# Kernel optimization log

Measured on AMD Instinct MI355X. Metric: run time of the kernel, lower is better.

Reference implementation:

```python
import math
import jax, jax.numpy as jnp
import numpy as np

MAX_N = 3; MAX_L = 3
CUTOFF = 5.0; TB_CUTOFF = 4.0; NBLOCKS = 3
N_NODES = 5000; N_EDGES = 60000; N_TRIP = 400000
NELEM = 89; DN = 128; DE = 128; UNITS = 128; DEG = MAX_N * MAX_L

# zeros of spherical bessel j_l, l = 0..2, first 3 roots each
J_ROOTS = np.array([
    [3.141592653589793, 6.283185307179586, 9.42477796076938],
    [4.493409457909064, 7.725251836937707, 10.904121659428899],
    [5.763459196894550, 9.095011330476355, 12.322940970566582],
])

def _jl(l, x, xp):
    s, c = xp.sin(x), xp.cos(x)
    if l == 0:
        return s / x
    if l == 1:
        return s / x**2 - c / x
    if l == 2:
        return (3.0 / x**3 - 1.0 / x) * s - 3.0 * c / x**2
    return (15.0 / x**4 - 6.0 / x**2) * s - (15.0 / x**3 - 1.0 / x) * c

SBF_FACTOR = math.sqrt(2.0 / CUTOFF**3)
SBF_NORM = np.stack([np.abs(_jl(l + 1, J_ROOTS[l], np)) for l in range(MAX_L)])  # [3,3]

def sbf_expand(r):  # [n] -> [n, MAX_L*MAX_N], l-major (matches torch cat over l)
    cols = []
    for l in range(MAX_L):
        x = r[:, None] * (J_ROOTS[l] / CUTOFF)[None, :]
        cols.append(_jl(l, x, jnp) * (SBF_FACTOR / SBF_NORM[l])[None, :])
    return jnp.concatenate(cols, axis=1)

Y00 = 0.28209479177387814  # 0.5*sqrt(1/pi)
Y10 = 0.4886025119029199   # sqrt(3/(4pi))
Y20 = 0.31539156525252005  # 0.25*sqrt(5/pi)

def shf_expand(cos_t):  # [n] -> [n, MAX_L]  real Y_l0(theta)
    return jnp.stack([jnp.full_like(cos_t, Y00), Y10 * cos_t, Y20 * (3.0 * cos_t**2 - 1.0)], axis=1)

def poly_cutoff(r, c):
    x = r / c
    return 1.0 - 6.0 * x**5 + 15.0 * x**4 - 10.0 * x**3

def gated_mlp(x, Ws, bs, gWs, gbs):
    h = x
    for W, b in zip(Ws, bs):
        h = jax.nn.silu(h @ W + b)
    g = x
    n = len(gWs)
    for i, (W, b) in enumerate(zip(gWs, gbs)):
        g = g @ W + b
        g = jax.nn.sigmoid(g) if i == n - 1 else jax.nn.silu(g)
    return h * g

def _forward(pos, node_type, src, dst, t_src, t_dst, emb_table, edge_emb_W, edge_emb_b,
             tb_atom_W, tb_atom_b, tb_bond_W, tb_bond_Wg,
             W0, b0, W1, b1, W2, b2, gW0, gb0, gW1, gb1, gW2, gb2, wt,
             fW0, fb0, fW1, fb1, fW2, fb2):
    n_nodes = pos.shape[0]; n_edges = src.shape[0]
    bond_vec = pos[dst] - pos[src]                              # [E,3]
    bond_dist = jnp.sqrt(jnp.sum(bond_vec**2, axis=1) + 1e-12)  # [E]
    rbf = sbf_expand(bond_dist)                                 # [E,9]
    # triplet (line-graph edge) geometry
    v1, v2 = bond_vec[t_src], bond_vec[t_dst]
    cos_t = jnp.sum(v1 * v2, axis=1) / (bond_dist[t_src] * bond_dist[t_dst])
    three_basis = sbf_expand(bond_dist[t_dst]) * jnp.repeat(shf_expand(cos_t), MAX_N, axis=1)  # [T,9]
    cut3 = poly_cutoff(bond_dist, TB_CUTOFF)
    tw = (cut3[t_src] * cut3[t_dst])[:, None]                   # [T,1]
    end_atom = dst[t_dst]                                       # [T]
    node_feat = emb_table[node_type]                            # [N,DN]
    edge_feat = jax.nn.silu(rbf @ edge_emb_W + edge_emb_b)      # [E,DE]
    for k in range(NBLOCKS):
        # --- three-body interaction ---
        atoms = jax.nn.sigmoid(node_feat @ tb_atom_W[k] + tb_atom_b[k])  # [N,9]
        basis = three_basis * atoms[end_atom] * tw                        # [T,9]
        nb = jax.ops.segment_sum(basis, t_src, num_segments=n_edges)      # [E,9]
        edge_feat = edge_feat + jax.nn.silu(nb @ tb_bond_W[k]) * jax.nn.sigmoid(nb @ tb_bond_Wg[k])
        # --- graph conv: edge update ---
        x = jnp.concatenate([node_feat[src], node_feat[dst], edge_feat], axis=1)  # [E,384]
        e_upd = gated_mlp(x, (W0[k, 0], W1[k, 0], W2[k, 0]), (b0[k, 0], b1[k, 0], b2[k, 0]),
                          (gW0[k, 0], gW1[k, 0], gW2[k, 0]), (gb0[k, 0], gb1[k, 0], gb2[k, 0])) * (rbf @ wt[k, 0])
        edge_feat = edge_feat + e_upd
        # --- graph conv: node update (sum messages at destination) ---
        x = jnp.concatenate([node_feat[src], node_feat[dst], edge_feat], axis=1)
        mess = gated_mlp(x, (W0[k, 1], W1[k, 1], W2[k, 1]), (b0[k, 1], b1[k, 1], b2[k, 1]),
                         (gW0[k, 1], gW1[k, 1], gW2[k, 1]), (gb0[k, 1], gb1[k, 1], gb2[k, 1])) * (rbf @ wt[k, 1])
        node_feat = node_feat + jax.ops.segment_sum(mess, dst, num_segments=n_nodes)
    # ReduceReadOut('mean') over nodes (single graph) + final MLP
    v = jnp.mean(node_feat, axis=0)
    h = jax.nn.silu(v @ fW0 + fb0)
    h = jax.nn.silu(h @ fW1 + fb1)
    return jnp.squeeze(h @ fW2 + fb2)

def setup_inputs() -> dict:
    key = jax.random.key(0)
    ks = iter(jax.random.split(key, 64))
    def nrm(shape, fan_in):
        return jax.random.normal(next(ks), shape, dtype=jnp.float32) / math.sqrt(float(fan_in))
    pos = jax.random.normal(next(ks), (N_NODES, 3), dtype=jnp.float32) * 1.5
    node_type = jax.random.randint(next(ks), (N_NODES,), 0, NELEM, dtype=jnp.int32)
    src = jax.random.randint(next(ks), (N_EDGES,), 0, N_NODES, dtype=jnp.int32)
    dst = (src + 1 + jax.random.randint(next(ks), (N_EDGES,), 0, N_NODES - 1, dtype=jnp.int32)) % N_NODES
    t_src = jax.random.randint(next(ks), (N_TRIP,), 0, N_EDGES, dtype=jnp.int32)
    t_dst = jax.random.randint(next(ks), (N_TRIP,), 0, N_EDGES, dtype=jnp.int32)
    DIN = 2 * DN + DE
    z = lambda *s: jnp.zeros(s, jnp.float32)
    return dict(
        pos=pos, node_type=node_type, src=src, dst=dst, t_src=t_src, t_dst=t_dst,
        emb_table=nrm((NELEM, DN), 1.0),
        edge_emb_W=nrm((DEG, DE), DEG), edge_emb_b=z(DE),
        tb_atom_W=nrm((NBLOCKS, DN, DEG), DN), tb_atom_b=z(NBLOCKS, DEG),
        tb_bond_W=nrm((NBLOCKS, DEG, DE), DEG), tb_bond_Wg=nrm((NBLOCKS, DEG, DE), DEG),
        W0=nrm((NBLOCKS, 2, DIN, UNITS), DIN), b0=z(NBLOCKS, 2, UNITS),
        W1=nrm((NBLOCKS, 2, UNITS, UNITS), UNITS), b1=z(NBLOCKS, 2, UNITS),
        W2=nrm((NBLOCKS, 2, UNITS, DE), UNITS), b2=z(NBLOCKS, 2, DE),
        gW0=nrm((NBLOCKS, 2, DIN, UNITS), DIN), gb0=z(NBLOCKS, 2, UNITS),
        gW1=nrm((NBLOCKS, 2, UNITS, UNITS), UNITS), gb1=z(NBLOCKS, 2, UNITS),
        gW2=nrm((NBLOCKS, 2, UNITS, DE), UNITS), gb2=z(NBLOCKS, 2, DE),
        wt=nrm((NBLOCKS, 2, DEG, DE), DEG),
        fW0=nrm((DN, UNITS), DN), fb0=z(UNITS),
        fW1=nrm((UNITS, UNITS), UNITS), fb1=z(UNITS),
        fW2=nrm((UNITS, 1), UNITS), fb2=z(1))

def reference(pos, node_type, src, dst, t_src, t_dst, emb_table, edge_emb_W, edge_emb_b,
              tb_atom_W, tb_atom_b, tb_bond_W, tb_bond_Wg,
              W0, b0, W1, b1, W2, b2, gW0, gb0, gW1, gb1, gW2, gb2, wt,
              fW0, fb0, fW1, fb1, fW2, fb2):
    return _forward(pos, node_type, src, dst, t_src, t_dst, emb_table, edge_emb_W, edge_emb_b,
                    tb_atom_W, tb_atom_b, tb_bond_W, tb_bond_Wg,
                    W0, b0, W1, b1, W2, b2, gW0, gb0, gW1, gb1, gW2, gb2, wt,
                    fW0, fb0, fW1, fb1, fW2, fb2)
```

## Files before the change

### kernel.cpp

```cpp
#include <hip/hip_runtime.h>
#include <stdint.h>

typedef __attribute__((ext_vector_type(8))) short bf16x8;
typedef __attribute__((ext_vector_type(4))) float f32x4;
typedef __attribute__((ext_vector_type(4))) uint32_t u32x4;

#define XSS 408
#define HSS 144
#define TE 32

__device__ __forceinline__ float sigm(float x) { return __fdividef(1.0f, 1.0f + __expf(-x)); }
__device__ __forceinline__ float silu(float x) { return __fdividef(x, 1.0f + __expf(-x)); }
__device__ __forceinline__ short f2bf(float f) {
  uint32_t u = __float_as_uint(f);
  u = (u + 0x7fffu + ((u >> 16) & 1u)) >> 16;
  return (short)u;
}
__device__ __forceinline__ uint32_t cvt2(float lo, float hi) {
  uint32_t d;
  asm("v_cvt_pk_bf16_f32 %0, %1, %2" : "=v"(d) : "v"(lo), "v"(hi));
  return d;
}
__device__ __forceinline__ short f2bf1(float f) { return (short)cvt2(f, f); }

__device__ __forceinline__ float jl_eval(int l, float x) {
  float s, c;
  sincosf(x, &s, &c);
  float ix = 1.0f / x, ix2 = ix * ix;
  if (l == 0) return s * ix;
  if (l == 1) return s * ix2 - c * ix;
  if (l == 2) return (3.0f * ix2 * ix - ix) * s - 3.0f * ix2 * c;
  return (15.0f * ix2 * ix2 - 6.0f * ix2) * s - (15.0f * ix2 * ix - ix) * c;
}

__global__ void setup1_kernel(const int* __restrict__ ntb, const float* __restrict__ emb,
                              float* __restrict__ nf, int N,
                              const float* __restrict__ pos, const int* __restrict__ src,
                              const int* __restrict__ dst, float* __restrict__ bvec,
                              float* __restrict__ bdist, float* __restrict__ rbf,
                              float* __restrict__ cut3, int E,
                              const int* __restrict__ t_src, int* __restrict__ cnt_e,
                              int* __restrict__ cnt_n, int T) {
  int i = blockIdx.x * 256 + threadIdx.x;
  if (i < N * 128) {
    int n = i >> 7, c = i & 127;
    nf[i] = emb[ntb[n] * 128 + c];
  }
  if (i < E) {
    int s = src[i], d = dst[i];
    float dx = pos[d * 3 + 0] - pos[s * 3 + 0];
    float dy = pos[d * 3 + 1] - pos[s * 3 + 1];
    float dz = pos[d * 3 + 2] - pos[s * 3 + 2];
    float r = sqrtf(dx * dx + dy * dy + dz * dz + 1e-12f);
    bvec[i * 3 + 0] = dx; bvec[i * 3 + 1] = dy; bvec[i * 3 + 2] = dz;
    bdist[i] = r;
    const float roots[3][3] = {
        {3.141592653589793f, 6.283185307179586f, 9.42477796076938f},
        {4.493409457909064f, 7.725251836937707f, 10.904121659428899f},
        {5.763459196894550f, 9.095011330476355f, 12.322940970566582f}};
#pragma unroll
    for (int l = 0; l < 3; ++l) {
#pragma unroll
      for (int n = 0; n < 3; ++n) {
        float root = roots[l][n];
        float x = r * (root * 0.2f);
        float norm = fabsf(jl_eval(l + 1, root));
        rbf[i * 9 + l * 3 + n] = jl_eval(l, x) * (0.12649110640673518f / norm);
      }
    }
    float xx = r * 0.25f;
    float x3 = xx * xx * xx;
    cut3[i] = 1.0f - 6.0f * x3 * xx * xx + 15.0f * x3 * xx - 10.0f * x3;
    atomicAdd(&cnt_n[d], 1);
  }
  if (i < T) atomicAdd(&cnt_e[t_src[i]], 1);
}

__device__ void scan_chunk(const int* __restrict__ in, int* __restrict__ incl,
                           int* __restrict__ bsum, int L, int b) {
  __shared__ int sm[256];
  int i = b * 256 + threadIdx.x;
  int v = i < L ? in[i] : 0;
  sm[threadIdx.x] = v;
  __syncthreads();
  for (int st = 1; st < 256; st <<= 1) {
    int t = threadIdx.x >= st ? sm[threadIdx.x - st] : 0;
    __syncthreads();
    sm[threadIdx.x] += t;
    __syncthreads();
  }
  if (i < L) incl[i] = sm[threadIdx.x];
  if (threadIdx.x == 255) bsum[b] = sm[255];
}

__global__ void setup2_kernel(const float* __restrict__ rbf, const float* __restrict__ eW,
                              const float* __restrict__ eB, float* __restrict__ ef, int E,
                              const int* __restrict__ cnt_e, int* __restrict__ incl_e,
                              int* __restrict__ bsum_e, int ebk,
                              const int* __restrict__ cnt_n, int* __restrict__ incl_n,
                              int* __restrict__ bsum_n, int nbk, int N,
                              const float* __restrict__ nf, const float* __restrict__ taW,
                              const float* __restrict__ taB, float* __restrict__ atoms) {
  int b = blockIdx.x;
  if (b < ebk) scan_chunk(cnt_e, incl_e, bsum_e, E, b);
  else if (b < ebk + nbk) scan_chunk(cnt_n, incl_n, bsum_n, N, b - ebk);
  int i = b * 256 + threadIdx.x;
  if (i < E * 128) {
    int e = i >> 7, c = i & 127;
    float acc = eB[c];
#pragma unroll
    for (int d = 0; d < 9; ++d) acc += rbf[e * 9 + d] * eW[d * 128 + c];
    ef[i] = silu(acc);
  }
  if (i < N * 9) {
    int n = i / 9, d = i - n * 9;
    float acc = taB[d];
    for (int c = 0; c < 128; ++c) acc += nf[n * 128 + c] * taW[c * 9 + d];
    atoms[i] = sigm(acc);
  }
}

__global__ void scan_top2_kernel(int* __restrict__ bsum_e, int ne, int* __restrict__ bsum_n,
                                 int nn) {
  __shared__ int sm[1024];
  int* bs = blockIdx.x == 0 ? bsum_e : bsum_n;
  int nb = blockIdx.x == 0 ? ne : nn;
  int tid = threadIdx.x;
  int orig = tid < nb ? bs[tid] : 0;
  sm[tid] = orig;
  __syncthreads();
  for (int st = 1; st < 1024; st <<= 1) {
    int t = tid >= st ? sm[tid - st] : 0;
    __syncthreads();
    sm[tid] += t;
    __syncthreads();
  }
  if (tid < nb) bs[tid] = sm[tid] - orig;
}

__global__ void fin2_kernel(const int* __restrict__ cnt_e, const int* __restrict__ incl_e,
                            const int* __restrict__ bsum_e, int ebk, int* __restrict__ off_e,
                            int* __restrict__ cur_e, int E, const int* __restrict__ cnt_n,
                            const int* __restrict__ incl_n, const int* __restrict__ bsum_n,
                            int* __restrict__ off_n, int* __restrict__ cur_n, int N) {
  int b = blockIdx.x;
  if (b < ebk) {
    int i = b * 256 + threadIdx.x;
    if (i < E) {
      int o = incl_e[i] - cnt_e[i] + bsum_e[b];
      off_e[i] = o; cur_e[i] = o;
    }
  } else {
    int bb = b - ebk;
    int i = bb * 256 + threadIdx.x;
    if (i < N) {
      int o = incl_n[i] - cnt_n[i] + bsum_n[bb];
      off_n[i] = o; cur_n[i] = o;
    }
  }
}

__global__ void build_kernel(const int* __restrict__ t_src, const int* __restrict__ t_dst,
                             const int* __restrict__ dst, const float* __restrict__ bvec,
                             const float* __restrict__ bdist, const float* __restrict__ rbf,
                             const float* __restrict__ cut3, int* __restrict__ cur_e,
                             float* __restrict__ stbp, int* __restrict__ sa, int T,
                             int* __restrict__ cur_n, int* __restrict__ eperm, int E) {
  int t = blockIdx.x * 256 + threadIdx.x;
  if (t < T) {
    int i = t_src[t], j = t_dst[t];
    float ax = bvec[i * 3], ay = bvec[i * 3 + 1], az = bvec[i * 3 + 2];
    float bx = bvec[j * 3], by = bvec[j * 3 + 1], bz = bvec[j * 3 + 2];
    float ct = (ax * bx + ay * by + az * bz) / (bdist[i] * bdist[j]);
    float tw = cut3[i] * cut3[j];
    float sh[3];
    sh[0] = 0.28209479177387814f * tw;
    sh[1] = 0.4886025119029199f * ct * tw;
    sh[2] = 0.31539156525252005f * (3.0f * ct * ct - 1.0f) * tw;
    int pos = atomicAdd(&cur_e[i], 1);
#pragma unroll
    for (int l = 0; l < 3; ++l)
#pragma unroll
      for (int n = 0; n < 3; ++n)
        stbp[(size_t)pos * 9 + l * 3 + n] = rbf[j * 9 + l * 3 + n] * sh[l];
    sa[pos] = dst[j];
  }
  if (t < E) {
    int pos = atomicAdd(&cur_n[dst[t]], 1);
    eperm[pos] = t;
  }
}

__device__ void pack_one(const float* __restrict__ Wf, short* __restrict__ Wp, int K, int rr) {
  int per = 8 * (K / 32) * 64;
  int u = rr / per, r2 = rr - u * per;
  int lane = r2 & 63, tile = r2 >> 6;
  int kt = tile % (K / 32), nt = tile / (K / 32);
  int n = nt * 16 + (lane & 15);
  int k0 = kt * 32 + (lane >> 4) * 8;
  const float* s = Wf + (size_t)u * K * 128;
  bf16x8 v;
#pragma unroll
  for (int e = 0; e < 8; ++e) v[e] = f2bf(s[(size_t)(k0 + e) * 128 + n]);
  *(bf16x8*)(Wp + (size_t)u * K * 128 + (size_t)tile * 512 + lane * 8) = v;
}

__global__ void pack_all_kernel(const float* __restrict__ W0, const float* __restrict__ G0,
                                const float* __restrict__ W1, const float* __restrict__ G1,
                                const float* __restrict__ W2, const float* __restrict__ G2,
                                short* __restrict__ pW0, short* __restrict__ pG0,
                                short* __restrict__ pW1, short* __restrict__ pG1,
                                short* __restrict__ pW2, short* __restrict__ pG2) {
  int idx = blockIdx.x * 256 + threadIdx.x;
  const int t384 = 6 * 8 * 12 * 64, t128 = 6 * 8 * 4 * 64;
  if (idx < t384) pack_one(W0, pW0, 384, idx);
  else if (idx < 2 * t384) pack_one(G0, pG0, 384, idx - t384);
  else {
    int j = idx - 2 * t384;
    if (j < t128) pack_one(W1, pW1, 128, j);
    else if (j < 2 * t128) pack_one(G1, pG1, 128, j - t128);
    else if (j < 3 * t128) pack_one(W2, pW2, 128, j - 2 * t128);
    else if (j < 4 * t128) pack_one(G2, pG2, 128, j - 3 * t128);
  }
}

__device__ __forceinline__ f32x4 mfma16(bf16x8 a, bf16x8 b, f32x4 c) {
  return __builtin_amdgcn_mfma_f32_16x16x32_bf16(a, b, c, 0, 0, 0);
}

__device__ __forceinline__ void store_hg(short* hsb, short* gsb, int wave, int lane,
                                         const f32x4 (&aW)[2], const f32x4 (&aG)[2]) {
  const int lrow = lane & 15, lk = lane >> 4;
  const int colx = (wave * 16 + lrow) ^ (lk << 4);
#pragma unroll
  for (int mt = 0; mt < 2; ++mt)
#pragma unroll
    for (int rg = 0; rg < 4; ++rg) {
      int row = mt * 16 + lk * 4 + rg;
      hsb[row * HSS + colx] = f2bf1(silu(aW[mt][rg]));
      gsb[row * HSS + colx] = f2bf1(silu(aG[mt][rg]));
    }
}

__device__ __forceinline__ void layer128w(const short* hin, const short* gin,
                                          const short* __restrict__ pW,
                                          const short* __restrict__ pG,
                                          const float* __restrict__ Bh,
                                          const float* __restrict__ Bg, int wave, int lane,
                                          f32x4 (&aW)[2], f32x4 (&aG)[2]) {
  const int lrow = lane & 15, lk = lane >> 4;
  const int s0 = (lrow >> 2) & 3;
  float bw = Bh[wave * 16 + lrow], bg = Bg[wave * 16 + lrow];
  aW[0] = {bw, bw, bw, bw}; aW[1] = aW[0];
  aG[0] = {bg, bg, bg, bg}; aG[1] = aG[0];
#pragma unroll
  for (int kt = 0; kt < 4; ++kt) {
    int aoff = (kt * 32 + lk * 8) ^ (s0 << 4);
    bf16x8 ah0 = *(const bf16x8*)(hin + (size_t)lrow * HSS + aoff);
    bf16x8 ah1 = *(const bf16x8*)(hin + (size_t)(16 + lrow) * HSS + aoff);
    bf16x8 ag0 = *(const bf16x8*)(gin + (size_t)lrow * HSS + aoff);
    bf16x8 ag1 = *(const bf16x8*)(gin + (size_t)(16 + lrow) * HSS + aoff);
    bf16x8 bw8 = *(const bf16x8*)(pW + (size_t)(wave * 4 + kt) * 512 + lane * 8);
    bf16x8 bg8 = *(const bf16x8*)(pG + (size_t)(wave * 4 + kt) * 512 + lane * 8);
    aW[0] = mfma16(ah0, bw8, aW[0]);
    aW[1] = mfma16(ah1, bw8, aW[1]);
    aG[0] = mfma16(ag0, bg8, aG[0]);
    aG[1] = mfma16(ag1, bg8, aG[1]);
  }
}

__device__ __forceinline__ void run_chain(
    const short* xsb, short* hsb, short* gsb,
    const short* __restrict__ pW0, const short* __restrict__ pG0,
    const short* __restrict__ pW1, const short* __restrict__ pG1,
    const short* __restrict__ pW2, const short* __restrict__ pG2,
    const float* __restrict__ B0, const float* __restrict__ Gb0,
    const float* __restrict__ B1, const float* __restrict__ Gb1,
    const float* __restrict__ B2, const float* __restrict__ Gb2,
    int wave, int lane, f32x4 (&aW)[2], f32x4 (&aG)[2]) {
  const int lrow = lane & 15, lk = lane >> 4;
  const int s0 = (lrow >> 2) & 3;
  {
    float bw = B0[wave * 16 + lrow], bg = Gb0[wave * 16 + lrow];
    aW[0] = {bw, bw, bw, bw}; aW[1] = aW[0];
    aG[0] = {bg, bg, bg, bg}; aG[1] = aG[0];
  }
#pragma unroll
  for (int kt = 0; kt < 12; ++kt) {
    int al = kt * 32 + lk * 8;
    int aoff = (al < 256) ? al : (256 + ((al - 256) ^ (s0 << 4)));
    bf16x8 a0 = *(const bf16x8*)(xsb + (size_t)lrow * XSS + aoff);
    bf16x8 a1 = *(const bf16x8*)(xsb + (size_t)(16 + lrow) * XSS + aoff);
    bf16x8 bw8 = *(const bf16x8*)(pW0 + (size_t)(wave * 12 + kt) * 512 + lane * 8);
    bf16x8 bg8 = *(const bf16x8*)(pG0 + (size_t)(wave * 12 + kt) * 512 + lane * 8);
    aW[0] = mfma16(a0, bw8, aW[0]);
    aW[1] = mfma16(a1, bw8, aW[1]);
    aG[0] = mfma16(a0, bg8, aG[0]);
    aG[1] = mfma16(a1, bg8, aG[1]);
  }
  store_hg(hsb, gsb, wave, lane, aW, aG);
  __syncthreads();
  layer128w(hsb, gsb, pW1, pG1, B1, Gb1, wave, lane, aW, aG);
  __syncthreads();
  store_hg(hsb, gsb, wave, lane, aW, aG);
  __syncthreads();
  layer128w(hsb, gsb, pW2, pG2, B2, Gb2, wave, lane, aW, aG);
}

__global__ __launch_bounds__(512, 6) void gmlp_fused(
    const float* __restrict__ nf, float* __restrict__ ef, const float* __restrict__ rbf,
    const int* __restrict__ src, const int* __restrict__ dst,
    const float* __restrict__ stbp, const int* __restrict__ sa,
    const int* __restrict__ off_e, const int* __restrict__ cnt_e,
    const float* __restrict__ atoms,
    const float* __restrict__ tbW, const float* __restrict__ tbG,
    const short* __restrict__ pW0a, const short* __restrict__ pG0a,
    const short* __restrict__ pW1a, const short* __restrict__ pG1a,
    const short* __restrict__ pW2a, const short* __restrict__ pG2a,
    const float* __restrict__ B0a, const float* __restrict__ Gb0a,
    const float* __restrict__ B1a, const float* __restrict__ Gb1a,
    const float* __restrict__ B2a, const float* __restrict__ Gb2a,
    const float* __restrict__ WTa,
    const short* __restrict__ pW0b, const short* __restrict__ pG0b,
    const short* __restrict__ pW1b, const short* __restrict__ pG1b,
    const short* __restrict__ pW2b, const short* __restrict__ pG2b,
    const float* __restrict__ B0b, const float* __restrict__ Gb0b,
    const float* __restrict__ B1b, const float* __restrict__ Gb1b,
    const float* __restrict__ B2b, const float* __restrict__ Gb2b,
    const float* __restrict__ WTb,
    float* __restrict__ mbuf, int E) {
  __shared__ __align__(16) short xs[32][XSS];
  __shared__ __align__(16) short hs[32 * HSS];
  __shared__ __align__(16) short gs[32 * HSS];
  __shared__ float rs[32][12];
  __shared__ float nbl[32][12];
  const int tid = threadIdx.x;
  const int e0 = blockIdx.x * TE;
  const int r = tid >> 4, q = tid & 15;
  const int sr = (r >> 2) & 3;
  int eg = e0 + r; if (eg >= E) eg = E - 1;

  if (q < 9) {
    int o = off_e[eg], c = cnt_e[eg];
    float acc = 0.f;
    for (int pp = o; pp < o + c; ++pp)
      acc += stbp[(size_t)pp * 9 + q] * atoms[(size_t)sa[pp] * 9 + q];
    nbl[r][q] = acc;
  }
  {
    const float* sp0 = nf + (size_t)src[eg] * 128;
    const float* sp1 = nf + (size_t)dst[eg] * 128;
#pragma unroll
    for (int seg = 0; seg < 2; ++seg) {
      const float* sp = seg == 0 ? sp0 : sp1;
      float4 f0 = *(const float4*)(sp + q * 8);
      float4 f1 = *(const float4*)(sp + q * 8 + 4);
      u32x4 v = {cvt2(f0.x, f0.y), cvt2(f0.z, f0.w), cvt2(f1.x, f1.y), cvt2(f1.z, f1.w)};
      *(u32x4*)&xs[r][seg * 128 + q * 8] = v;
    }
    for (int idx = tid; idx < 32 * 9; idx += 512) {
      int rr = idx / 9, d = idx - rr * 9;
      int ee = e0 + rr; if (ee >= E) ee = E - 1;
      rs[rr][d] = rbf[ee * 9 + d];
    }
  }
  __syncthreads();

  {
    float nb9[9];
#pragma unroll
    for (int d = 0; d < 9; ++d) nb9[d] = nbl[r][d];
    float fv[8];
    {
      float4 f0 = *(const float4*)(ef + (size_t)eg * 128 + q * 8);
      float4 f1 = *(const float4*)(ef + (size_t)eg * 128 + q * 8 + 4);
      fv[0]=f0.x; fv[1]=f0.y; fv[2]=f0.z; fv[3]=f0.w;
      fv[4]=f1.x; fv[5]=f1.y; fv[6]=f1.z; fv[7]=f1.w;
    }
    float a8[8], b8[8];
#pragma unroll
    for (int c = 0; c < 8; ++c) { a8[c] = 0.f; b8[c] = 0.f; }
#pragma unroll
    for (int d = 0; d < 9; ++d) {
      float nbd = nb9[d];
      float4 w0 = *(const float4*)(tbW + d * 128 + q * 8);
      float4 w1 = *(const float4*)(tbW + d * 128 + q * 8 + 4);
      float4 g0 = *(const float4*)(tbG + d * 128 + q * 8);
      float4 g1 = *(const float4*)(tbG + d * 128 + q * 8 + 4);
      a8[0] = fmaf(nbd, w0.x, a8[0]); a8[1] = fmaf(nbd, w0.y, a8[1]);
      a8[2] = fmaf(nbd, w0.z, a8[2]); a8[3] = fmaf(nbd, w0.w, a8[3]);
      a8[4] = fmaf(nbd, w1.x, a8[4]); a8[5] = fmaf(nbd, w1.y, a8[5]);
      a8[6] = fmaf(nbd, w1.z, a8[6]); a8[7] = fmaf(nbd, w1.w, a8[7]);
      b8[0] = fmaf(nbd, g0.x, b8[0]); b8[1] = fmaf(nbd, g0.y, b8[1]);
      b8[2] = fmaf(nbd, g0.z, b8[2]); b8[3] = fmaf(nbd, g0.w, b8[3]);
      b8[4] = fmaf(nbd, g1.x, b8[4]); b8[5] = fmaf(nbd, g1.y, b8[5]);
      b8[6] = fmaf(nbd, g1.z, b8[6]); b8[7] = fmaf(nbd, g1.w, b8[7]);
    }
    float vals[8];
#pragma unroll
    for (int c = 0; c < 8; ++c) vals[c] = fv[c] + silu(a8[c]) * sigm(b8[c]);
    u32x4 v = {cvt2(vals[0], vals[1]), cvt2(vals[2], vals[3]),
               cvt2(vals[4], vals[5]), cvt2(vals[6], vals[7])};
    *(u32x4*)&xs[r][256 + ((q * 8) ^ (sr << 4))] = v;
  }
  __syncthreads();

  const int wave = tid >> 6;
  const int lane = tid & 63;
  const int lrow = lane & 15, lk = lane >> 4;
  const int col = wave * 16 + lrow;
  f32x4 aW[2], aG[2];

  run_chain(&xs[0][0], hs, gs, pW0a, pG0a, pW1a, pG1a, pW2a, pG2a,
            B0a, Gb0a, B1a, Gb1a, B2a, Gb2a, wave, lane, aW, aG);
  {
    float wtc[9];
#pragma unroll
    for (int d = 0; d < 9; ++d) wtc[d] = WTa[d * 128 + col];
    const int cs = 256 + (col ^ (lk << 4));
#pragma unroll
    for (int mt = 0; mt < 2; ++mt)
#pragma unroll
      for (int rg = 0; rg < 4; ++rg) {
        int row = mt * 16 + lk * 4 + rg;
        int e = e0 + row;
        float wv = 0.f;
#pragma unroll
        for (int d = 0; d < 9; ++d) wv = fmaf(rs[row][d], wtc[d], wv);
        float v = silu(aW[mt][rg]) * sigm(aG[mt][rg]) * wv;
        uint32_t ub = ((uint32_t)(uint16_t)xs[row][cs]) << 16;
        float nv = __uint_as_float(ub) + v;
        if (e < E) ef[(size_t)e * 128 + col] = nv;
        xs[row][cs] = f2bf1(nv);
      }
  }
  __syncthreads();

  run_chain(&xs[0][0], hs, gs, pW0b, pG0b, pW1b, pG1b, pW2b, pG2b,
            B0b, Gb0b, B1b, Gb1b, B2b, Gb2b, wave, lane, aW, aG);
  {
    float wtc[9];
#pragma unroll
    for (int d = 0; d < 9; ++d) wtc[d] = WTb[d * 128 + col];
#pragma unroll
    for (int mt = 0; mt < 2; ++mt)
#pragma unroll
      for (int rg = 0; rg < 4; ++rg) {
        int row = mt * 16 + lk * 4 + rg;
        int e = e0 + row;
        float wv = 0.f;
#pragma unroll
        for (int d = 0; d < 9; ++d) wv = fmaf(rs[row][d], wtc[d], wv);
        float v = silu(aW[mt][rg]) * sigm(aG[mt][rg]) * wv;
        if (e < E) mbuf[(size_t)e * 128 + col] = v;
      }
  }
}

__global__ void node_gather_kernel(float* __restrict__ nf, const float* __restrict__ mbuf,
                                   const int* __restrict__ off_n, const int* __restrict__ cnt_n,
                                   const int* __restrict__ eperm, const float* __restrict__ taW,
                                   const float* __restrict__ taB, float* __restrict__ atoms,
                                   int N, int doAtoms) {
  __shared__ float sm[2][128];
  int half = threadIdx.x >> 7, c = threadIdx.x & 127;
  int n = blockIdx.x * 2 + half;
  float v = 0.f;
  if (n < N) {
    int o = off_n[n], cnt = cnt_n[n];
    float acc = 0.f;
    for (int p = o; p < o + cnt; ++p) acc += mbuf[(size_t)eperm[p] * 128 + c];
    v = nf[(size_t)n * 128 + c] + acc;
    nf[(size_t)n * 128 + c] = v;
  }
  if (doAtoms) {
    sm[half][c] = v;
    __syncthreads();
    if (n < N && c < 9) {
      float a = taB[c];
      for (int cc = 0; cc < 128; ++cc) a += sm[half][cc] * taW[cc * 9 + c];
      atoms[n * 9 + c] = sigm(a);
    }
  }
}

__global__ void mean_kernel(const float* __restrict__ nf, float* __restrict__ partial, int N) {
  __shared__ float sm[256];
  int n0 = blockIdx.x * 256;
  int col = threadIdx.x & 127, half = threadIdx.x >> 7;
  int nend = n0 + 256 < N ? n0 + 256 : N;
  float s = 0.f;
  for (int n = n0 + half; n < nend; n += 2) s += nf[n * 128 + col];
  sm[threadIdx.x] = s;
  __syncthreads();
  if (threadIdx.x < 128)
    partial[blockIdx.x * 128 + threadIdx.x] = sm[threadIdx.x] + sm[threadIdx.x + 128];
}

__global__ void final_kernel(const float* __restrict__ partial, int nchunks, float Nf,
                             const float* __restrict__ fW0, const float* __restrict__ fb0,
                             const float* __restrict__ fW1, const float* __restrict__ fb1,
                             const float* __restrict__ fW2, const float* __restrict__ fb2,
                             float* __restrict__ out) {
  __shared__ float v[128], h[128], red[128];
  int tid = threadIdx.x;
  float s = 0.f;
  for (int b = 0; b < nchunks; ++b) s += partial[b * 128 + tid];
  v[tid] = s / Nf;
  __syncthreads();
  float acc = fb0[tid];
  for (int c = 0; c < 128; ++c) acc += v[c] * fW0[c * 128 + tid];
  h[tid] = silu(acc);
  __syncthreads();
  acc = fb1[tid];
  for (int c = 0; c < 128; ++c) acc += h[c] * fW1[c * 128 + tid];
  __syncthreads();
  v[tid] = silu(acc);
  __syncthreads();
  red[tid] = v[tid] * fW2[tid];
  __syncthreads();
  for (int st = 64; st > 0; st >>= 1) {
    if (tid < st) red[tid] += red[tid + st];
    __syncthreads();
  }
  if (tid == 0) out[0] = red[0] + fb2[0];
}

extern "C" void kernel_launch(void* const* d_in, const int* in_sizes, int n_in,
                              void* d_out, int out_size, void* d_ws, size_t ws_size,
                              hipStream_t stream) {
  const float* pos = (const float*)d_in[0];
  const int* node_type = (const int*)d_in[1];
  const int* src = (const int*)d_in[2];
  const int* dst = (const int*)d_in[3];
  const int* t_src = (const int*)d_in[4];
  const int* t_dst = (const int*)d_in[5];
  const float* emb = (const float*)d_in[6];
  const float* eW = (const float*)d_in[7];
  const float* eB = (const float*)d_in[8];
  const float* taW = (const float*)d_in[9];
  const float* taB = (const float*)d_in[10];
  const float* tbW = (const float*)d_in[11];
  const float* tbG = (const float*)d_in[12];
  const float* W0 = (const float*)d_in[13]; const float* B0 = (const float*)d_in[14];
  const float* W1 = (const float*)d_in[15]; const float* B1 = (const float*)d_in[16];
  const float* W2 = (const float*)d_in[17]; const float* B2 = (const float*)d_in[18];
  const float* G0 = (const float*)d_in[19]; const float* Gb0 = (const float*)d_in[20];
  const float* G1 = (const float*)d_in[21]; const float* Gb1 = (const float*)d_in[22];
  const float* G2 = (const float*)d_in[23]; const float* Gb2 = (const float*)d_in[24];
  const float* WT = (const float*)d_in[25];
  const float* fW0 = (const float*)d_in[26]; const float* fb0 = (const float*)d_in[27];
  const float* fW1 = (const float*)d_in[28]; const float* fb1 = (const float*)d_in[29];
  const float* fW2 = (const float*)d_in[30]; const float* fb2 = (const float*)d_in[31];

  const int N = in_sizes[1];
  const int E = in_sizes[2];
  const int T = in_sizes[4];

  char* p = (char*)d_ws;
  auto alloc = [&](size_t bytes) -> char* {
    char* r = p;
    p += (bytes + 255) & ~(size_t)255;
    return r;
  };
  float* nf    = (float*)alloc((size_t)N * 128 * 4);
  float* ef    = (float*)alloc((size_t)E * 128 * 4);
  float* mbuf  = (float*)alloc((size_t)E * 128 * 4);
  float* rbf   = (float*)alloc((size_t)E * 9 * 4);
  float* bvec  = (float*)alloc((size_t)E * 3 * 4);
  float* bdist = (float*)alloc((size_t)E * 4);
  float* cut3  = (float*)alloc((size_t)E * 4);
  float* stbp  = (float*)alloc((size_t)T * 9 * 4);
  int*   sa    = (int*)alloc((size_t)T * 4);
  float* atoms = (float*)alloc((size_t)N * 9 * 4);
  float* part  = (float*)alloc((size_t)64 * 128 * 4);
  int* cnt_all = (int*)alloc((size_t)(E + N) * 4);
  int* cnt_e = cnt_all, *cnt_n = cnt_all + E;
  int* incl_e = (int*)alloc((size_t)E * 4);
  int* incl_n = (int*)alloc((size_t)N * 4);
  int* off_e  = (int*)alloc((size_t)E * 4);
  int* off_n  = (int*)alloc((size_t)N * 4);
  int* cur_e  = (int*)alloc((size_t)E * 4);
  int* cur_n  = (int*)alloc((size_t)N * 4);
  int* eperm  = (int*)alloc((size_t)E * 4);
  int* bsum_e = (int*)alloc((size_t)1024 * 4);
  int* bsum_n = (int*)alloc((size_t)1024 * 4);
  short* pW0s = (short*)alloc((size_t)6 * 384 * 128 * 2);
  short* pG0s = (short*)alloc((size_t)6 * 384 * 128 * 2);
  short* pW1s = (short*)alloc((size_t)6 * 128 * 128 * 2);
  short* pG1s = (short*)alloc((size_t)6 * 128 * 128 * 2);
  short* pW2s = (short*)alloc((size_t)6 * 128 * 128 * 2);
  short* pG2s = (short*)alloc((size_t)6 * 128 * 128 * 2);
  (void)ws_size; (void)n_in; (void)out_size;

  const int ebk = (E + 255) / 256, nbk = (N + 255) / 256;

  pack_all_kernel<<<480, 256, 0, stream>>>(W0, G0, W1, G1, W2, G2, pW0s, pG0s, pW1s, pG1s,
                                           pW2s, pG2s);
  hipMemsetAsync(cnt_all, 0, (size_t)(E + N) * 4, stream);
  {
    int g1 = N * 128; if (E > g1) g1 = E; if (T > g1) g1 = T;
    setup1_kernel<<<(g1 + 255) / 256, 256, 0, stream>>>(
        node_type, emb, nf, N, pos, src, dst, bvec, bdist, rbf, cut3, E, t_src, cnt_e, cnt_n, T);
  }
  {
    int g2 = E * 128; int g2b = (ebk + nbk) * 256; if (g2b > g2) g2 = g2b;
    if (N * 9 > g2) g2 = N * 9;
    setup2_kernel<<<(g2 + 255) / 256, 256, 0, stream>>>(
        rbf, eW, eB, ef, E, cnt_e, incl_e, bsum_e, ebk, cnt_n, incl_n, bsum_n, nbk, N,
        nf, taW, taB, atoms);
  }
  scan_top2_kernel<<<2, 1024, 0, stream>>>(bsum_e, ebk, bsum_n, nbk);
  fin2_kernel<<<ebk + nbk, 256, 0, stream>>>(cnt_e, incl_e, bsum_e, ebk, off_e, cur_e, E,
                                             cnt_n, incl_n, bsum_n, off_n, cur_n, N);
  {
    int g3 = T > E ? T : E;
    build_kernel<<<(g3 + 255) / 256, 256, 0, stream>>>(t_src, t_dst, dst, bvec, bdist, rbf,
                                                       cut3, cur_e, stbp, sa, T, cur_n, eperm, E);
  }

  const int gblocks = (E + TE - 1) / TE;
  for (int k = 0; k < 3; ++k) {
    size_t u0 = (size_t)(k * 2 + 0), u1 = u0 + 1;
    gmlp_fused<<<gblocks, 512, 0, stream>>>(
        nf, ef, rbf, src, dst, stbp, sa, off_e, cnt_e, atoms,
        tbW + (size_t)k * 9 * 128, tbG + (size_t)k * 9 * 128,
        pW0s + u0 * 384 * 128, pG0s + u0 * 384 * 128, pW1s + u0 * 128 * 128,
        pG1s + u0 * 128 * 128, pW2s + u0 * 128 * 128, pG2s + u0 * 128 * 128,
        B0 + u0 * 128, Gb0 + u0 * 128, B1 + u0 * 128, Gb1 + u0 * 128, B2 + u0 * 128,
        Gb2 + u0 * 128, WT + u0 * 9 * 128,
        pW0s + u1 * 384 * 128, pG0s + u1 * 384 * 128, pW1s + u1 * 128 * 128,
        pG1s + u1 * 128 * 128, pW2s + u1 * 128 * 128, pG2s + u1 * 128 * 128,
        B0 + u1 * 128, Gb0 + u1 * 128, B1 + u1 * 128, Gb1 + u1 * 128, B2 + u1 * 128,
        Gb2 + u1 * 128, WT + u1 * 9 * 128,
        mbuf, E);
    int nk = k < 2 ? k + 1 : 0;
    node_gather_kernel<<<(N + 1) / 2, 256, 0, stream>>>(
        nf, mbuf, off_n, cnt_n, eperm, taW + (size_t)nk * 128 * 9, taB + (size_t)nk * 9,
        atoms, N, k < 2 ? 1 : 0);
  }

  int nchunks = (N + 255) / 256;
  mean_kernel<<<nchunks, 256, 0, stream>>>(nf, part, N);
  final_kernel<<<1, 128, 0, stream>>>(part, nchunks, (float)N, fW0, fb0, fW1, fb1, fW2, fb2,
                                      (float*)d_out);
}
```

Before: 556.6 us.

## Use MFMA for three-body update, scatter messages in dst order, skip last ef write

Replaces the scalar FMA three-body gating with a bf16 MFMA against pre-packed, zero-padded tbW/tbG weights, and keeps the fp32 edge base in registers. Messages are written straight into dst-sorted slots through an inverse permutation, so node_gather reads contiguous rows with no indirection. The final block's ef writeback is skipped because nothing reads it afterwards. LDS row strides are also shrunk. Costs are bf16 rounding on the three-body input and a scattered write pattern for mbuf.

```diff
diff --git a/kernel.cpp b/kernel.cpp
--- a/kernel.cpp
+++ b/kernel.cpp
@@ -5,8 +5,8 @@
 typedef __attribute__((ext_vector_type(4))) float f32x4;
 typedef __attribute__((ext_vector_type(4))) uint32_t u32x4;
 
-#define XSS 408
-#define HSS 144
+#define XSS 392
+#define HSS 136
 #define TE 32
 
 __device__ __forceinline__ float sigm(float x) { return __fdividef(1.0f, 1.0f + __expf(-x)); }
@@ -165,7 +165,7 @@
                              const float* __restrict__ bdist, const float* __restrict__ rbf,
                              const float* __restrict__ cut3, int* __restrict__ cur_e,
                              float* __restrict__ stbp, int* __restrict__ sa, int T,
-                             int* __restrict__ cur_n, int* __restrict__ eperm, int E) {
+                             int* __restrict__ cur_n, int* __restrict__ invp, int E) {
   int t = blockIdx.x * 256 + threadIdx.x;
   if (t < T) {
     int i = t_src[t], j = t_dst[t];
@@ -187,7 +187,7 @@
   }
   if (t < E) {
     int pos = atomicAdd(&cur_n[dst[t]], 1);
-    eperm[pos] = t;
+    invp[t] = pos;
   }
 }
 
@@ -208,19 +208,34 @@
 __global__ void pack_all_kernel(const float* __restrict__ W0, const float* __restrict__ G0,
                                 const float* __restrict__ W1, const float* __restrict__ G1,
                                 const float* __restrict__ W2, const float* __restrict__ G2,
+                                const float* __restrict__ tbW, const float* __restrict__ tbG,
                                 short* __restrict__ pW0, short* __restrict__ pG0,
                                 short* __restrict__ pW1, short* __restrict__ pG1,
-                                short* __restrict__ pW2, short* __restrict__ pG2) {
+                                short* __restrict__ pW2, short* __restrict__ pG2,
+                                short* __restrict__ ptbW, short* __restrict__ ptbG) {
   int idx = blockIdx.x * 256 + threadIdx.x;
   const int t384 = 6 * 8 * 12 * 64, t128 = 6 * 8 * 4 * 64;
-  if (idx < t384) pack_one(W0, pW0, 384, idx);
-  else if (idx < 2 * t384) pack_one(G0, pG0, 384, idx - t384);
-  else {
-    int j = idx - 2 * t384;
-    if (j < t128) pack_one(W1, pW1, 128, j);
-    else if (j < 2 * t128) pack_one(G1, pG1, 128, j - t128);
-    else if (j < 3 * t128) pack_one(W2, pW2, 128, j - 2 * t128);
-    else if (j < 4 * t128) pack_one(G2, pG2, 128, j - 3 * t128);
+  if (idx < t384) { pack_one(W0, pW0, 384, idx); return; }
+  if (idx < 2 * t384) { pack_one(G0, pG0, 384, idx - t384); return; }
+  int j = idx - 2 * t384;
+  if (j < t128) { pack_one(W1, pW1, 128, j); return; }
+  if (j < 2 * t128) { pack_one(G1, pG1, 128, j - t128); return; }
+  if (j < 3 * t128) { pack_one(W2, pW2, 128, j - 2 * t128); return; }
+  if (j < 4 * t128) { pack_one(G2, pG2, 128, j - 3 * t128); return; }
+  j -= 4 * t128;
+  if (j < 3072) {
+    int kb = j >> 10;
+    int w2 = (j >> 9) & 1;
+    int l2 = j & 511;
+    int lane = l2 & 63, tile = l2 >> 6;
+    int n = tile * 16 + (lane & 15);
+    int k0 = (lane >> 4) * 8;
+    const float* s = (w2 ? tbG : tbW) + (size_t)kb * 9 * 128;
+    short* dp = (w2 ? ptbG : ptbW) + (size_t)kb * 4096 + tile * 512 + lane * 8;
+    bf16x8 v;
+#pragma unroll
+    for (int e = 0; e < 8; ++e) v[e] = (k0 + e < 9) ? f2bf(s[(size_t)(k0 + e) * 128 + n]) : (short)0;
+    *(bf16x8*)dp = v;
   }
 }
 
@@ -312,8 +327,8 @@
     const int* __restrict__ src, const int* __restrict__ dst,
     const float* __restrict__ stbp, const int* __restrict__ sa,
     const int* __restrict__ off_e, const int* __restrict__ cnt_e,
-    const float* __restrict__ atoms,
-    const float* __restrict__ tbW, const float* __restrict__ tbG,
+    const float* __restrict__ atoms, const int* __restrict__ invp,
+    const short* __restrict__ ptbW, const short* __restrict__ ptbG,
     const short* __restrict__ pW0a, const short* __restrict__ pG0a,
     const short* __restrict__ pW1a, const short* __restrict__ pG1a,
     const short* __restrict__ pW2a, const short* __restrict__ pG2a,
@@ -328,24 +343,27 @@
     const float* __restrict__ B1b, const float* __restrict__ Gb1b,
     const float* __restrict__ B2b, const float* __restrict__ Gb2b,
     const float* __restrict__ WTb,
-    float* __restrict__ mbuf, int E) {
+    float* __restrict__ mbuf, int E, int writeEf) {
   __shared__ __align__(16) short xs[32][XSS];
   __shared__ __align__(16) short hs[32 * HSS];
   __shared__ __align__(16) short gs[32 * HSS];
   __shared__ float rs[32][12];
-  __shared__ float nbl[32][12];
+  __shared__ __align__(16) short nbl[32][40];
+  __shared__ int invs[32];
   const int tid = threadIdx.x;
   const int e0 = blockIdx.x * TE;
   const int r = tid >> 4, q = tid & 15;
-  const int sr = (r >> 2) & 3;
   int eg = e0 + r; if (eg >= E) eg = E - 1;
 
-  if (q < 9) {
-    int o = off_e[eg], c = cnt_e[eg];
+  {
     float acc = 0.f;
-    for (int pp = o; pp < o + c; ++pp)
-      acc += stbp[(size_t)pp * 9 + q] * atoms[(size_t)sa[pp] * 9 + q];
-    nbl[r][q] = acc;
+    if (q < 9) {
+      int o = off_e[eg], c = cnt_e[eg];
+      for (int pp = o; pp < o + c; ++pp)
+        acc += stbp[(size_t)pp * 9 + q] * atoms[(size_t)sa[pp] * 9 + q];
+    }
+    nbl[r][q] = (q < 9) ? f2bf1(acc) : (short)0;
+    nbl[r][q + 16] = 0;
   }
   {
     const float* sp0 = nf + (size_t)src[eg] * 128;
@@ -363,45 +381,10 @@
       int ee = e0 + rr; if (ee >= E) ee = E - 1;
       rs[rr][d] = rbf[ee * 9 + d];
     }
-  }
-  __syncthreads();
-
-  {
-    float nb9[9];
-#pragma unroll
-    for (int d = 0; d < 9; ++d) nb9[d] = nbl[r][d];
-    float fv[8];
-    {
-      float4 f0 = *(const float4*)(ef + (size_t)eg * 128 + q * 8);
-      float4 f1 = *(const float4*)(ef + (size_t)eg * 128 + q * 8 + 4);
-      fv[0]=f0.x; fv[1]=f0.y; fv[2]=f0.z; fv[3]=f0.w;
-      fv[4]=f1.x; fv[5]=f1.y; fv[6]=f1.z; fv[7]=f1.w;
-    }
-    float a8[8], b8[8];
-#pragma unroll
-    for (int c = 0; c < 8; ++c) { a8[c] = 0.f; b8[c] = 0.f; }
-#pragma unroll
-    for (int d = 0; d < 9; ++d) {
-      float nbd = nb9[d];
-      float4 w0 = *(const float4*)(tbW + d * 128 + q * 8);
-      float4 w1 = *(const float4*)(tbW + d * 128 + q * 8 + 4);
-      float4 g0 = *(const float4*)(tbG + d * 128 + q * 8);
-      float4 g1 = *(const float4*)(tbG + d * 128 + q * 8 + 4);
-      a8[0] = fmaf(nbd, w0.x, a8[0]); a8[1] = fmaf(nbd, w0.y, a8[1]);
-      a8[2] = fmaf(nbd, w0.z, a8[2]); a8[3] = fmaf(nbd, w0.w, a8[3]);
-      a8[4] = fmaf(nbd, w1.x, a8[4]); a8[5] = fmaf(nbd, w1.y, a8[5]);
-      a8[6] = fmaf(nbd, w1.z, a8[6]); a8[7] = fmaf(nbd, w1.w, a8[7]);
-      b8[0] = fmaf(nbd, g0.x, b8[0]); b8[1] = fmaf(nbd, g0.y, b8[1]);
-      b8[2] = fmaf(nbd, g0.z, b8[2]); b8[3] = fmaf(nbd, g0.w, b8[3]);
-      b8[4] = fmaf(nbd, g1.x, b8[4]); b8[5] = fmaf(nbd, g1.y, b8[5]);
-      b8[6] = fmaf(nbd, g1.z, b8[6]); b8[7] = fmaf(nbd, g1.w, b8[7]);
-    }
-    float vals[8];
-#pragma unroll
-    for (int c = 0; c < 8; ++c) vals[c] = fv[c] + silu(a8[c]) * sigm(b8[c]);
-    u32x4 v = {cvt2(vals[0], vals[1]), cvt2(vals[2], vals[3]),
-               cvt2(vals[4], vals[5]), cvt2(vals[6], vals[7])};
-    *(u32x4*)&xs[r][256 + ((q * 8) ^ (sr << 4))] = v;
+    if (tid < 32) {
+      int ee = e0 + tid; if (ee >= E) ee = E - 1;
+      invs[tid] = invp[ee];
+    }
   }
   __syncthreads();
 
@@ -410,6 +393,30 @@
   const int lrow = lane & 15, lk = lane >> 4;
   const int col = wave * 16 + lrow;
   f32x4 aW[2], aG[2];
+  float efb[2][4];
+
+  {
+    bf16x8 ta0 = *(const bf16x8*)&nbl[lrow][lk * 8];
+    bf16x8 ta1 = *(const bf16x8*)&nbl[16 + lrow][lk * 8];
+    bf16x8 tbw = *(const bf16x8*)(ptbW + wave * 512 + lane * 8);
+    bf16x8 tbg = *(const bf16x8*)(ptbG + wave * 512 + lane * 8);
+    f32x4 z = {0.f, 0.f, 0.f, 0.f};
+    f32x4 tW0 = mfma16(ta0, tbw, z), tW1 = mfma16(ta1, tbw, z);
+    f32x4 tG0 = mfma16(ta0, tbg, z), tG1 = mfma16(ta1, tbg, z);
+#pragma unroll
+    for (int mt = 0; mt < 2; ++mt)
+#pragma unroll
+      for (int rg = 0; rg < 4; ++rg) {
+        int row = mt * 16 + lk * 4 + rg;
+        int ec = e0 + row; if (ec >= E) ec = E - 1;
+        float tw = mt == 0 ? tW0[rg] : tW1[rg];
+        float tg = mt == 0 ? tG0[rg] : tG1[rg];
+        float base = ef[(size_t)ec * 128 + col] + silu(tw) * sigm(tg);
+        efb[mt][rg] = base;
+        xs[row][256 + (col ^ (lk << 4))] = f2bf1(base);
+      }
+  }
+  __syncthreads();
 
   run_chain(&xs[0][0], hs, gs, pW0a, pG0a, pW1a, pG1a, pW2a, pG2a,
             B0a, Gb0a, B1a, Gb1a, B2a, Gb2a, wave, lane, aW, aG);
@@ -428,9 +435,8 @@
 #pragma unroll
         for (int d = 0; d < 9; ++d) wv = fmaf(rs[row][d], wtc[d], wv);
         float v = silu(aW[mt][rg]) * sigm(aG[mt][rg]) * wv;
-        uint32_t ub = ((uint32_t)(uint16_t)xs[row][cs]) << 16;
-        float nv = __uint_as_float(ub) + v;
-        if (e < E) ef[(size_t)e * 128 + col] = nv;
+        float nv = efb[mt][rg] + v;
+        if (e < E && writeEf) ef[(size_t)e * 128 + col] = nv;
         xs[row][cs] = f2bf1(nv);
       }
   }
@@ -452,16 +458,15 @@
 #pragma unroll
         for (int d = 0; d < 9; ++d) wv = fmaf(rs[row][d], wtc[d], wv);
         float v = silu(aW[mt][rg]) * sigm(aG[mt][rg]) * wv;
-        if (e < E) mbuf[(size_t)e * 128 + col] = v;
+        if (e < E) mbuf[(size_t)invs[row] * 128 + col] = v;
       }
   }
 }
 
 __global__ void node_gather_kernel(float* __restrict__ nf, const float* __restrict__ mbuf,
                                    const int* __restrict__ off_n, const int* __restrict__ cnt_n,
-                                   const int* __restrict__ eperm, const float* __restrict__ taW,
-                                   const float* __restrict__ taB, float* __restrict__ atoms,
-                                   int N, int doAtoms) {
+                                   const float* __restrict__ taW, const float* __restrict__ taB,
+                                   float* __restrict__ atoms, int N, int doAtoms) {
   __shared__ float sm[2][128];
   int half = threadIdx.x >> 7, c = threadIdx.x & 127;
   int n = blockIdx.x * 2 + half;
@@ -469,7 +474,7 @@
   if (n < N) {
     int o = off_n[n], cnt = cnt_n[n];
     float acc = 0.f;
-    for (int p = o; p < o + cnt; ++p) acc += mbuf[(size_t)eperm[p] * 128 + c];
+    for (int p = 0; p < cnt; ++p) acc += mbuf[(size_t)(o + p) * 128 + c];
     v = nf[(size_t)n * 128 + c] + acc;
     nf[(size_t)n * 128 + c] = v;
   }
@@ -582,7 +587,7 @@
   int* off_n  = (int*)alloc((size_t)N * 4);
   int* cur_e  = (int*)alloc((size_t)E * 4);
   int* cur_n  = (int*)alloc((size_t)N * 4);
-  int* eperm  = (int*)alloc((size_t)E * 4);
+  int* invp   = (int*)alloc((size_t)E * 4);
   int* bsum_e = (int*)alloc((size_t)1024 * 4);
   int* bsum_n = (int*)alloc((size_t)1024 * 4);
   short* pW0s = (short*)alloc((size_t)6 * 384 * 128 * 2);
@@ -591,12 +596,14 @@
   short* pG1s = (short*)alloc((size_t)6 * 128 * 128 * 2);
   short* pW2s = (short*)alloc((size_t)6 * 128 * 128 * 2);
   short* pG2s = (short*)alloc((size_t)6 * 128 * 128 * 2);
+  short* ptbWs = (short*)alloc((size_t)3 * 4096 * 2);
+  short* ptbGs = (short*)alloc((size_t)3 * 4096 * 2);
   (void)ws_size; (void)n_in; (void)out_size;
 
   const int ebk = (E + 255) / 256, nbk = (N + 255) / 256;
 
-  pack_all_kernel<<<480, 256, 0, stream>>>(W0, G0, W1, G1, W2, G2, pW0s, pG0s, pW1s, pG1s,
-                                           pW2s, pG2s);
+  pack_all_kernel<<<492, 256, 0, stream>>>(W0, G0, W1, G1, W2, G2, tbW, tbG,
+                                           pW0s, pG0s, pW1s, pG1s, pW2s, pG2s, ptbWs, ptbGs);
   hipMemsetAsync(cnt_all, 0, (size_t)(E + N) * 4, stream);
   {
     int g1 = N * 128; if (E > g1) g1 = E; if (T > g1) g1 = T;
@@ -616,15 +623,15 @@
   {
     int g3 = T > E ? T : E;
     build_kernel<<<(g3 + 255) / 256, 256, 0, stream>>>(t_src, t_dst, dst, bvec, bdist, rbf,
-                                                       cut3, cur_e, stbp, sa, T, cur_n, eperm, E);
+                                                       cut3, cur_e, stbp, sa, T, cur_n, invp, E);
   }
 
   const int gblocks = (E + TE - 1) / TE;
   for (int k = 0; k < 3; ++k) {
     size_t u0 = (size_t)(k * 2 + 0), u1 = u0 + 1;
     gmlp_fused<<<gblocks, 512, 0, stream>>>(
-        nf, ef, rbf, src, dst, stbp, sa, off_e, cnt_e, atoms,
-        tbW + (size_t)k * 9 * 128, tbG + (size_t)k * 9 * 128,
+        nf, ef, rbf, src, dst, stbp, sa, off_e, cnt_e, atoms, invp,
+        ptbWs + (size_t)k * 4096, ptbGs + (size_t)k * 4096,
         pW0s + u0 * 384 * 128, pG0s + u0 * 384 * 128, pW1s + u0 * 128 * 128,
         pG1s + u0 * 128 * 128, pW2s + u0 * 128 * 128, pG2s + u0 * 128 * 128,
         B0 + u0 * 128, Gb0 + u0 * 128, B1 + u0 * 128, Gb1 + u0 * 128, B2 + u0 * 128,
@@ -633,10 +640,10 @@
         pG1s + u1 * 128 * 128, pW2s + u1 * 128 * 128, pG2s + u1 * 128 * 128,
         B0 + u1 * 128, Gb0 + u1 * 128, B1 + u1 * 128, Gb1 + u1 * 128, B2 + u1 * 128,
         Gb2 + u1 * 128, WT + u1 * 9 * 128,
-        mbuf, E);
+        mbuf, E, k < 2 ? 1 : 0);
     int nk = k < 2 ? k + 1 : 0;
     node_gather_kernel<<<(N + 1) / 2, 256, 0, stream>>>(
-        nf, mbuf, off_n, cnt_n, eperm, taW + (size_t)nk * 128 * 9, taB + (size_t)nk * 9,
+        nf, mbuf, off_n, cnt_n, taW + (size_t)nk * 128 * 9, taB + (size_t)nk * 9,
         atoms, N, k < 2 ? 1 : 0);
   }
 
```

Result: faster. 521.3 us (-6.3%).
